# Kernel optimization log

Measured on AMD Instinct MI355X. Metric: run time of the kernel, lower is better.

Reference implementation:

```python
import jax, jax.numpy as jnp
import numpy as np

B, S, D, H = 8, 512, 1024, 16
DH = D // H
GAMMA = 0.1      # kl_gamma
KL_EPS = 1e-10
LN_EPS = 1e-5
SCALE = 1.0 / np.sqrt(DH).astype(np.float32)


def setup_inputs() -> dict:
    key = jax.random.key(0)
    ks = iter(jax.random.split(key, 32))
    rnd = lambda shape, s: jax.random.normal(next(ks), shape, jnp.float32) * s
    inp = {
        'title_features': rnd((B, S, D), 1.0),
        'content_features': rnd((B, S, D), 1.0),
    }
    for pre in ('t2c', 'c2t'):
        # small Q/K weights + bias 1.0 keep row-means of scores positive (log is defined)
        inp[pre + '_wq'] = rnd((D, D), 0.02); inp[pre + '_bq'] = jnp.ones((D,), jnp.float32)
        inp[pre + '_wk'] = rnd((D, D), 0.02); inp[pre + '_bk'] = jnp.ones((D,), jnp.float32)
        inp[pre + '_wv'] = rnd((D, D), 0.02); inp[pre + '_bv'] = jnp.zeros((D,), jnp.float32)
        inp[pre + '_wo'] = rnd((D, D), 0.02); inp[pre + '_bo'] = jnp.zeros((D,), jnp.float32)
    inp['gate_w'] = rnd((2 * D, D), 0.02)
    inp['gate_b'] = jnp.zeros((D,), jnp.float32)
    inp['ln_g'] = jnp.ones((D,), jnp.float32)
    inp['ln_b'] = jnpps = jnp.zeros((D,), jnp.float32)
    inp['ln_b'] = jnp.zeros((D,), jnp.float32)
    return inp


def _daa(q_in, k_in, v_in, wq, bq, wk, bk, wv, bv, wo, bo):
    """DivergenceAlignedAttention forward (eval mode, use_uniform_target=False)."""
    Bq, Sq, _ = q_in.shape
    Sk = k_in.shape[1]
    Q = (q_in @ wq + bq).reshape(Bq, Sq, H, DH)
    K = (k_in @ wk + bk).reshape(Bq, Sk, H, DH)
    V = (v_in @ wv + bv).reshape(Bq, Sk, H, DH)
    scores = jnp.einsum('bqhd,bkhd->bhqk', Q, K) * SCALE           # [B,H,Sq,Sk]
    tgt = jnp.mean(scores, axis=-1, keepdims=True)                 # row mean
    scores = scores + GAMMA * jnp.log(tgt + KL_EPS)                # fused KL term
    attn = jax.nn.softmax(scores, axis=-1)
    ctx = jnp.einsum('bhqk,bkhd->bqhd', attn, V).reshape(Bq, Sq, D)
    return ctx @ wo + bo


def _layer_norm(x, g, b):
    mu = jnp.mean(x, axis=-1, keepdims=True)
    var = jnp.mean(jnp.square(x - mu), axis=-1, keepdims=True)
    return g * (x - mu) / jnp.sqrt(var + LN_EPS) + b


def reference(title_features, content_features,
              t2c_wq, t2c_bq, t2c_wk, t2c_bk, t2c_wv, t2c_bv, t2c_wo, t2c_bo,
              c2t_wq, c2t_bq, c2t_wk, c2t_bk, c2t_wv, c2t_bv, c2t_wo, c2t_bo,
              gate_w, gate_b, ln_g, ln_b):
    t2c = _daa(content_features, title_features, title_features,
               t2c_wq, t2c_bq, t2c_wk, t2c_bk, t2c_wv, t2c_bv, t2c_wo, t2c_bo)
    c2t = _daa(title_features, content_features, content_features,
               c2t_wq, c2t_bq, c2t_wk, c2t_bk, c2t_wv, c2t_bv, c2t_wo, c2t_bo)
    gate_t = jax.nn.sigmoid(jnp.concatenate([title_features, t2c], axis=-1) @ gate_w + gate_b)
    gate_c = jax.nn.sigmoid(jnp.concatenate([content_features, c2t], axis=-1) @ gate_w + gate_b)
    fused_title = _layer_norm(gate_t * title_features + (1.0 - gate_t) * t2c, ln_g, ln_b)
    fused_content = _layer_norm(gate_c * content_features + (1.0 - gate_c) * c2t, ln_g, ln_b)
    return (fused_title, fused_content)
```

## Files before the change

kernel.cpp:

```cpp
#include <hip/hip_runtime.h>
#include <cstdint>
#include <cstddef>

typedef unsigned short ushort_t;
typedef unsigned int u32;
typedef __attribute__((ext_vector_type(8))) short bf16x8;
typedef __attribute__((ext_vector_type(4))) float f32x4;
typedef __attribute__((ext_vector_type(4))) unsigned short u16x4;

#define DEV static __device__ __forceinline__

DEV ushort_t f2bf(float f) {
  u32 x = __float_as_uint(f);
  x += 0x7fff + ((x >> 16) & 1);
  return (ushort_t)(x >> 16);
}
DEV float bf2f(ushort_t u) { return __uint_as_float(((u32)u) << 16); }

DEV void gload16(const ushort_t* g, ushort_t* l) {
  __builtin_amdgcn_global_load_lds(
      (const __attribute__((address_space(1))) void*)g,
      (__attribute__((address_space(3))) void*)l, 16, 0, 0);
}


__global__ __launch_bounds__(256) void cvt_inputs(
    const float* __restrict__ xa, const float* __restrict__ xb,
    ushort_t* __restrict__ oa, ushort_t* __restrict__ ob) {
  int i = blockIdx.x * 256 + threadIdx.x;
  f32x4 va = ((const f32x4*)xa)[i];
  f32x4 vb = ((const f32x4*)xb)[i];
  u16x4 ua, ub;
#pragma unroll
  for (int j = 0; j < 4; ++j) { ua[j] = f2bf(va[j]); ub[j] = f2bf(vb[j]); }
  ((u16x4*)oa)[i] = ua;
  ((u16x4*)ob)[i] = ub;
}

struct Src11 { const float* p[11]; };

__global__ __launch_bounds__(256) void transpose_cvt(
    Src11 srcs, ushort_t* __restrict__ WTall, ushort_t* __restrict__ WgT,
    ushort_t* __restrict__ WoBF) {
  const int z = blockIdx.z;
  if (z != 8 && blockIdx.y >= 32) return;
  const float* src = srcs.p[z];
  int tx = threadIdx.x & 31, ty = threadIdx.x >> 5;
  int n0 = blockIdx.x << 5, k0 = blockIdx.y << 5;
  if (z >= 9) {
    ushort_t* dst = WoBF + ((size_t)(z - 9) << 20);
#pragma unroll
    for (int i = 0; i < 4; ++i) {
      size_t off = (size_t)(k0 + ty + i * 8) * 1024 + n0 + tx;
      dst[off] = f2bf(src[off]);
    }
    return;
  }
  const int K = (z == 8) ? 2048 : 1024;
  ushort_t* dst = (z == 8) ? WgT : WTall + ((size_t)z << 20);
  __shared__ float t[32][33];
#pragma unroll
  for (int i = 0; i < 4; ++i)
    t[ty + i * 8][tx] = src[(size_t)(k0 + ty + i * 8) * 1024 + n0 + tx];
  __syncthreads();
#pragma unroll
  for (int i = 0; i < 4; ++i)
    dst[(size_t)(n0 + ty + i * 8) * K + k0 + tx] = f2bf(t[tx][ty + i * 8]);
}

__global__ __launch_bounds__(256) void gb2_kernel(
    const float* __restrict__ bo0, const float* __restrict__ bo1,
    const ushort_t* __restrict__ WgT, float* __restrict__ gb2) {
  const int wgl = blockIdx.x * 4 + (threadIdx.x >> 6);
  const int lane = threadIdx.x & 63;
  const int dir = wgl >> 10, n = wgl & 1023;
  const float* bo = dir ? bo1 : bo0;
  const ushort_t* wrow = WgT + ((size_t)n << 11) + 1024 + (lane << 4);
  float s = 0.f;
#pragma unroll
  for (int j = 0; j < 16; ++j) s += bo[(lane << 4) + j] * bf2f(wrow[j]);
#pragma unroll
  for (int d = 1; d < 64; d <<= 1) s += __shfl_xor(s, d, 64);
  if (lane == 0) gb2[wgl] = s;
}

__global__ __launch_bounds__(256, 3) void gemm_wp(
    const ushort_t* __restrict__ WgT, const ushort_t* __restrict__ WoBF,
    ushort_t* __restrict__ WpT) {
  __shared__ ushort_t As[128 * 64];
  __shared__ ushort_t Bs[128 * 64];
  const int tid = threadIdx.x;
  const int w = tid >> 6, lane = tid & 63;
  const int g = lane >> 4, c = lane & 15;
  const int wm = (w >> 1) << 6, wn = (w & 1) << 6;
  const int m0 = blockIdx.x << 7, n0 = blockIdx.y << 7;
  const int group = m0 >> 10;
  const int csw = (lane & 7) ^ (lane >> 3);

  f32x4 acc[4][4];
#pragma unroll
  for (int i = 0; i < 4; ++i)
#pragma unroll
    for (int j = 0; j < 4; ++j) acc[i][j] = f32x4{0.f, 0.f, 0.f, 0.f};

  for (int k0 = 0; k0 < 1024; k0 += 64) {
#pragma unroll
    for (int i = 0; i < 4; ++i) {
      const int chunk = (w << 2) + i;
      const int row = (chunk << 3) + (lane >> 3);
      gload16(WgT + ((size_t)((m0 + row) & 1023) << 11) + 1024 + k0 + (csw << 3),
              &As[(size_t)chunk << 9]);
      gload16(WoBF + ((size_t)group << 20) + ((size_t)(n0 + row) << 10) + k0 + (csw << 3),
              &Bs[(size_t)chunk << 9]);
    }
    __syncthreads();
    const int cg = c & 7;
#pragma unroll
    for (int ks = 0; ks < 2; ++ks) {
      bf16x8 af[4], bfr[4];
#pragma unroll
      for (int mi = 0; mi < 4; ++mi)
        af[mi] = *(const bf16x8*)&As[((wm + mi * 16 + c) << 6) +
                                     ((((ks << 2) | g) ^ cg) << 3)];
#pragma unroll
      for (int ni = 0; ni < 4; ++ni)
        bfr[ni] = *(const bf16x8*)&Bs[((wn + ni * 16 + c) << 6) +
                                      ((((ks << 2) | g) ^ cg) << 3)];
#pragma unroll
      for (int mi = 0; mi < 4; ++mi)
#pragma unroll
        for (int ni = 0; ni < 4; ++ni)
          acc[mi][ni] = __builtin_amdgcn_mfma_f32_16x16x32_bf16(
              af[mi], bfr[ni], acc[mi][ni], 0, 0, 0);
    }
    __syncthreads();
  }
#pragma unroll
  for (int ni = 0; ni < 4; ++ni) {
    const int n = n0 + wn + ni * 16 + c;
#pragma unroll
    for (int mi = 0; mi < 4; ++mi) {
      const int mb = m0 + wm + mi * 16 + (g << 2);
      f32x4 a = acc[mi][ni];
#pragma unroll
      for (int r = 0; r < 4; ++r)
        WpT[((size_t)group << 20) + ((size_t)((mb + r) & 1023) << 10) + n] = f2bf(a[r]);
    }
  }
}

enum { M_QKVG = 0, M_OG = 1 };
struct Bias8 { const float* p[8]; };

template <int MODE>
__global__ __launch_bounds__(256, 3) void gemm_kernel(
    const ushort_t* __restrict__ Aa, const ushort_t* __restrict__ Ab,
    const ushort_t* __restrict__ WTall, const ushort_t* __restrict__ WgT,
    const ushort_t* __restrict__ WpT, Bias8 bt, const float* __restrict__ gb2,
    ushort_t* __restrict__ outQ, ushort_t* __restrict__ gt) {
  __shared__ ushort_t As[128 * 64];
  __shared__ ushort_t Bs[128 * 64];
  const int tid = threadIdx.x;
  const int w = tid >> 6, lane = tid & 63;
  const int g = lane >> 4, c = lane & 15;
  const int wm = (w >> 1) << 6, wn = (w & 1) << 6;
  const int bid = (int)blockIdx.x;
  const int xcd = bid & 7, idx = bid >> 3;
  const int mt = (xcd << 3) + (idx & 7), nt = idx >> 3;
  const int m0 = mt << 7, n0 = nt << 7;
  const int group = m0 >> 12;
  const int nch = n0 >> 10;
  const int csw = (lane & 7) ^ (lane >> 3);

  const ushort_t* Asrc = (MODE == M_QKVG)
      ? ((group ? Ab : Aa) + ((size_t)(m0 & 4095) << 10))
      : (Aa + ((size_t)m0 << 10));

  const ushort_t* Bb;
  int bstr, bidx = -1;
  if (MODE == M_QKVG) {
    if (nch < 3) {
      bidx = group * 3 + nch;
      Bb = WTall + ((size_t)bidx << 20) + ((size_t)(n0 & 1023) << 10);
      bstr = 1024;
    } else {
      Bb = WgT + ((size_t)(n0 & 1023) << 11);
      bstr = 2048;
    }
  } else {
    if (nch == 0) {
      Bb = WTall + ((size_t)(6 + group) << 20) + ((size_t)n0 << 10);
      bstr = 1024;
    } else {
      Bb = WpT + ((size_t)group << 20) + ((size_t)(n0 & 1023) << 10);
      bstr = 1024;
    }
  }

  f32x4 acc[4][4];
#pragma unroll
  for (int i = 0; i < 4; ++i)
#pragma unroll
    for (int j = 0; j < 4; ++j) acc[i][j] = f32x4{0.f, 0.f, 0.f, 0.f};

  for (int k0 = 0; k0 < 1024; k0 += 64) {
#pragma unroll
    for (int i = 0; i < 4; ++i) {
      const int chunk = (w << 2) + i;
      const int row = (chunk << 3) + (lane >> 3);
      gload16(Asrc + ((size_t)row << 10) + k0 + (csw << 3), &As[(size_t)chunk << 9]);
      gload16(Bb + (size_t)row * bstr + k0 + (csw << 3), &Bs[(size_t)chunk << 9]);
    }
    __syncthreads();
    const int cg = c & 7;
#pragma unroll
    for (int ks = 0; ks < 2; ++ks) {
      bf16x8 af[4], bfr[4];
#pragma unroll
      for (int mi = 0; mi < 4; ++mi)
        af[mi] = *(const bf16x8*)&As[((wm + mi * 16 + c) << 6) +
                                     ((((ks << 2) | g) ^ cg) << 3)];
#pragma unroll
      for (int ni = 0; ni < 4; ++ni)
        bfr[ni] = *(const bf16x8*)&Bs[((wn + ni * 16 + c) << 6) +
                                      ((((ks << 2) | g) ^ cg) << 3)];
#pragma unroll
      for (int mi = 0; mi < 4; ++mi)
#pragma unroll
        for (int ni = 0; ni < 4; ++ni)
          acc[mi][ni] = __builtin_amdgcn_mfma_f32_16x16x32_bf16(
              af[mi], bfr[ni], acc[mi][ni], 0, 0, 0);
    }
    __syncthreads();
  }

#pragma unroll
  for (int ni = 0; ni < 4; ++ni) {
    const int n = n0 + wn + ni * 16 + c;
    const int nloc = n & 1023;
    float bv;
    if (MODE == M_QKVG)
      bv = (nch < 3) ? bt.p[bidx][nloc]
                     : bt.p[6][nloc] + gb2[(group << 10) + nloc];
    else
      bv = (nch == 0) ? bt.p[group][nloc] : 0.f;
#pragma unroll
    for (int mi = 0; mi < 4; ++mi) {
      const int mb = m0 + wm + mi * 16 + (g << 2);
      f32x4 a = acc[mi][ni];
      if (MODE == M_QKVG) {
        if (nch < 3) {
          const int mrow = mb & 4095, b = mrow >> 9, s = mrow & 511;
          const int h = nloc >> 6, d = nloc & 63;
          ushort_t* base = outQ + ((size_t)bidx << 22);
          if (bidx == 1 || bidx == 5) {
            u16x4 o;
#pragma unroll
            for (int r = 0; r < 4; ++r) o[r] = f2bf(a[r] + bv);
            *(u16x4*)&base[(((size_t)((b * 16 + h) * 64 + d)) << 9) + s] = o;
          } else {
#pragma unroll
            for (int r = 0; r < 4; ++r)
              base[(((size_t)((b * 16 + h) * 512 + s + r)) << 6) + d] = f2bf(a[r] + bv);
          }
        } else {
#pragma unroll
          for (int r = 0; r < 4; ++r)
            gt[((size_t)(mb + r) << 10) + nloc] = f2bf(a[r] + bv);
        }
      } else {
        if (nch == 0) {
#pragma unroll
          for (int r = 0; r < 4; ++r)
            outQ[((size_t)(mb + r) << 10) + nloc] = f2bf(a[r] + bv);
        } else {
#pragma unroll
          for (int r = 0; r < 4; ++r)
            gt[((size_t)(mb + r) << 10) + nloc] = f2bf(a[r]);
        }
      }
    }
  }
}

__global__ __launch_bounds__(256, 2) void attn_kernel(
    const ushort_t* __restrict__ QKV, ushort_t* __restrict__ ctx) {
  __shared__ ushort_t kv[2][8192];
  const int tid = threadIdx.x, w = tid >> 6, lane = tid & 63;
  const int g = lane >> 4, c = lane & 15, c7 = c & 7;
  const int bid = (int)blockIdx.x;
  const int wid = (bid & 7) * 256 + (bid >> 3);
  const int dir = wid >> 10;
  const int bh = (wid >> 3) & 127, qt = wid & 7;
  const int q0 = (qt << 6) + (w << 4);
  const int qs = dir ? 2 : 3, ks = dir ? 4 : 0, vs = dir ? 5 : 1;
  const ushort_t* Qb = QKV + ((size_t)qs << 22) + ((size_t)bh << 15);
  const ushort_t* Kb = QKV + ((size_t)ks << 22) + ((size_t)bh << 15);
  const ushort_t* Vb = QKV + ((size_t)vs << 22) + ((size_t)bh << 15);

  auto stageK = [&](int b, int kc) {
#pragma unroll
    for (int i = 0; i < 4; ++i) {
      int idx = tid + (i << 8);
      int r = idx >> 3, sl = idx & 7;
      int cs = sl ^ (r & 7);
      gload16(Kb + (((size_t)((kc << 7) + r)) << 6) + (cs << 3), &kv[b][idx << 3]);
    }
  };
  auto stageV = [&](int b, int vc) {
#pragma unroll
    for (int i = 0; i < 4; ++i) {
      int idx = tid + (i << 8);
      int r = idx >> 4, sl = idx & 15;
      int cs = sl ^ (r & 15);
      gload16(Vb + ((size_t)r << 9) + (vc << 7) + (cs << 3), &kv[b][idx << 3]);
    }
  };

  bf16x8 qf0 = *(const bf16x8*)&Qb[((q0 + c) << 6) + (g << 3)];
  bf16x8 qf1 = *(const bf16x8*)&Qb[((q0 + c) << 6) + 32 + (g << 3)];

  f32x4 s[32];
  float mx = -1e30f;
  int buf = 0;
  stageK(0, 0);
  __syncthreads();
#pragma unroll
  for (int kc = 0; kc < 4; ++kc) {
    if (kc < 3) stageK(buf ^ 1, kc + 1);
    __builtin_amdgcn_s_setprio(1);
#pragma unroll
    for (int t = 0; t < 8; ++t) {
      const ushort_t* base = &kv[buf][((t << 4) + c) << 6];
      bf16x8 a0 = *(const bf16x8*)&base[(g ^ c7) << 3];
      bf16x8 a1 = *(const bf16x8*)&base[((4 | g) ^ c7) << 3];
      f32x4 z = {0.f, 0.f, 0.f, 0.f};
      z = __builtin_amdgcn_mfma_f32_16x16x32_bf16(a0, qf0, z, 0, 0, 0);
      z = __builtin_amdgcn_mfma_f32_16x16x32_bf16(a1, qf1, z, 0, 0, 0);
      s[kc * 8 + t] = z;
      mx = fmaxf(mx, fmaxf(fmaxf(z[0], z[1]), fmaxf(z[2], z[3])));
    }
    __builtin_amdgcn_s_setprio(0);
    __syncthreads();
    buf ^= 1;
  }
  stageV(0, 0);
  buf = 0;

  mx = fmaxf(mx, __shfl_xor(mx, 16, 64));
  mx = fmaxf(mx, __shfl_xor(mx, 32, 64));
  const float SC = 0.125f;
  float sum = 0.f;
#pragma unroll
  for (int t = 0; t < 32; ++t) {
#pragma unroll
    for (int r = 0; r < 4; ++r) {
      float p = __expf((s[t][r] - mx) * SC);
      s[t][r] = p;
      sum += p;
    }
  }
  sum += __shfl_xor(sum, 16, 64);
  sum += __shfl_xor(sum, 32, 64);
  const float inv = 1.0f / sum;

  f32x4 pacc[4];
#pragma unroll
  for (int dt = 0; dt < 4; ++dt) pacc[dt] = f32x4{0.f, 0.f, 0.f, 0.f};
  const int s1 = ((g & 1) << 5) + c;
  const int s2 = s1 + 16;
  const bool hi = (g >> 1) != 0;
  __syncthreads();
#pragma unroll
  for (int vc = 0; vc < 4; ++vc) {
    if (vc < 3) stageV(buf ^ 1, vc + 1);
#pragma unroll
    for (int t2l = 0; t2l < 4; ++t2l) {
      const int t2 = (vc << 2) + t2l;
      u32 A0 = ((u32)f2bf(s[2 * t2][1]) << 16) | f2bf(s[2 * t2][0]);
      u32 A1p = ((u32)f2bf(s[2 * t2][3]) << 16) | f2bf(s[2 * t2][2]);
      u32 B0 = ((u32)f2bf(s[2 * t2 + 1][1]) << 16) | f2bf(s[2 * t2 + 1][0]);
      u32 B1 = ((u32)f2bf(s[2 * t2 + 1][3]) << 16) | f2bf(s[2 * t2 + 1][2]);
      u32 xA0 = (u32)__shfl((int)A0, s1, 64), xA1 = (u32)__shfl((int)A1p, s1, 64);
      u32 xB0 = (u32)__shfl((int)B0, s1, 64), xB1 = (u32)__shfl((int)B1, s1, 64);
      u32 yA0 = (u32)__shfl((int)A0, s2, 64), yA1 = (u32)__shfl((int)A1p, s2, 64);
      u32 yB0 = (u32)__shfl((int)B0, s2, 64), yB1 = (u32)__shfl((int)B1, s2, 64);
      union { bf16x8 v; u32 wd[4]; } pb;
      pb.wd[0] = hi ? xB0 : xA0;
      pb.wd[1] = hi ? xB1 : xA1;
      pb.wd[2] = hi ? yB0 : yA0;
      pb.wd[3] = hi ? yB1 : yA1;
      __builtin_amdgcn_s_setprio(1);
#pragma unroll
      for (int dt = 0; dt < 4; ++dt) {
        bf16x8 av = *(const bf16x8*)
            &kv[buf][(((dt << 4) + c) << 7) + ((((t2l << 2) | g) ^ c) << 3)];
        pacc[dt] = __builtin_amdgcn_mfma_f32_16x16x32_bf16(av, pb.v, pacc[dt], 0, 0, 0);
      }
      __builtin_amdgcn_s_setprio(0);
    }
    __syncthreads();
    buf ^= 1;
  }

  const int b = bh >> 4, h = bh & 15;
  size_t obase = ((size_t)dir << 22) + ((size_t)(b * 512 + q0 + c) << 10) + (h << 6);
#pragma unroll
  for (int dt = 0; dt < 4; ++dt) {
    u16x4 o;
#pragma unroll
    for (int r = 0; r < 4; ++r) o[r] = f2bf(pacc[dt][r] * inv);
    *(u16x4*)&ctx[obase + (dt << 4) + (g << 2)] = o;
  }
}

__global__ __launch_bounds__(256) void fuse_ln(
    const float* __restrict__ xt, const float* __restrict__ xc,
    const ushort_t* __restrict__ ao, const ushort_t* __restrict__ gt,
    const ushort_t* __restrict__ gp,
    const float* __restrict__ lng, const float* __restrict__ lnb,
    float* __restrict__ out) {
  const int row = blockIdx.x, dir = row >> 12, r = row & 4095;
  const float* x = (dir ? xc : xt) + ((size_t)r << 10);
  const ushort_t* a = ao + ((size_t)row << 10);
  const ushort_t* g1 = gt + ((size_t)row << 10);
  const ushort_t* g2 = gp + ((size_t)row << 10);
  float* o = out + ((size_t)row << 10);
  const int t = threadIdx.x, w = t >> 6, lane = t & 63;
  f32x4 xv = ((const f32x4*)x)[t];
  u16x4 av = ((const u16x4*)a)[t];
  u16x4 gv = ((const u16x4*)g1)[t];
  u16x4 pv = ((const u16x4*)g2)[t];
  f32x4 f;
  float sm = 0.f, sq = 0.f;
#pragma unroll
  for (int j = 0; j < 4; ++j) {
    float gate = 1.f / (1.f + __expf(-(bf2f(gv[j]) + bf2f(pv[j]))));
    float fv = gate * xv[j] + (1.f - gate) * bf2f(av[j]);
    f[j] = fv; sm += fv; sq += fv * fv;
  }
#pragma unroll
  for (int d = 1; d < 64; d <<= 1) {
    sm += __shfl_xor(sm, d, 64);
    sq += __shfl_xor(sq, d, 64);
  }
  __shared__ float ps[8];
  if (lane == 0) { ps[w] = sm; ps[4 + w] = sq; }
  __syncthreads();
  sm = ps[0] + ps[1] + ps[2] + ps[3];
  sq = ps[4] + ps[5] + ps[6] + ps[7];
  const float mu = sm * (1.f / 1024.f);
  const float var = sq * (1.f / 1024.f) - mu * mu;
  const float rstd = rsqrtf(var + 1e-5f);
  f32x4 lg = ((const f32x4*)lng)[t], lb = ((const f32x4*)lnb)[t];
  f32x4 ov;
#pragma unroll
  for (int j = 0; j < 4; ++j) ov[j] = lg[j] * (f[j] - mu) * rstd + lb[j];
  ((f32x4*)o)[t] = ov;
}

extern "C" void kernel_launch(void* const* d_in, const int* in_sizes, int n_in,
                              void* d_out, int out_size, void* d_ws, size_t ws_size,
                              hipStream_t stream) {
  (void)in_sizes; (void)n_in; (void)out_size; (void)ws_size;
  const float* title = (const float*)d_in[0];
  const float* content = (const float*)d_in[1];

  char* ws = (char*)d_ws;
  const size_t MB = 1u << 20;
  ushort_t* Xt    = (ushort_t*)(ws + 0 * MB);
  ushort_t* Xc    = (ushort_t*)(ws + 8 * MB);
  ushort_t* ctx   = (ushort_t*)(ws + 0 * MB);
  ushort_t* WTall = (ushort_t*)(ws + 16 * MB);
  ushort_t* WgT   = (ushort_t*)(ws + 32 * MB);
  ushort_t* QKV   = (ushort_t*)(ws + 36 * MB);
  ushort_t* ao    = (ushort_t*)(ws + 36 * MB);
  ushort_t* gpart = (ushort_t*)(ws + 52 * MB);
  ushort_t* gt    = (ushort_t*)(ws + 84 * MB);
  ushort_t* WoBF  = (ushort_t*)(ws + 100 * MB);
  ushort_t* WpT   = (ushort_t*)(ws + 104 * MB);
  float*    gb2   = (float*)   (ws + 108 * MB);

  cvt_inputs<<<4096, 256, 0, stream>>>(title, content, Xt, Xc);

  Src11 srcs;
  srcs.p[0] = (const float*)d_in[4];  srcs.p[1] = (const float*)d_in[6];
  srcs.p[2] = (const float*)d_in[10]; srcs.p[3] = (const float*)d_in[2];
  srcs.p[4] = (const float*)d_in[12]; srcs.p[5] = (const float*)d_in[14];
  srcs.p[6] = (const float*)d_in[8];  srcs.p[7] = (const float*)d_in[16];
  srcs.p[8] = (const float*)d_in[18];
  srcs.p[9] = (const float*)d_in[8];  srcs.p[10] = (const float*)d_in[16];
  transpose_cvt<<<dim3(32, 64, 11), 256, 0, stream>>>(srcs, WTall, WgT, WoBF);

  gb2_kernel<<<512, 256, 0, stream>>>((const float*)d_in[9], (const float*)d_in[17],
                                      WgT, gb2);
  gemm_wp<<<dim3(16, 8), 256, 0, stream>>>(WgT, WoBF, WpT);

  Bias8 bq;
  bq.p[0] = (const float*)d_in[5];  bq.p[1] = (const float*)d_in[7];
  bq.p[2] = (const float*)d_in[11]; bq.p[3] = (const float*)d_in[3];
  bq.p[4] = (const float*)d_in[13]; bq.p[5] = (const float*)d_in[15];
  bq.p[6] = (const float*)d_in[19]; bq.p[7] = nullptr;
  gemm_kernel<M_QKVG><<<2048, 256, 0, stream>>>(Xt, Xc, WTall, WgT, WpT, bq, gb2,
                                                QKV, gt);

  attn_kernel<<<2048, 256, 0, stream>>>(QKV, ctx);

  Bias8 bo;
  bo.p[0] = (const float*)d_in[9]; bo.p[1] = (const float*)d_in[17];
  for (int i = 2; i < 8; ++i) bo.p[i] = nullptr;
  gemm_kernel<M_OG><<<1024, 256, 0, stream>>>(ctx, nullptr, WTall, WgT, WpT, bo, gb2,
                                              ao, gpart);

  fuse_ln<<<8192, 256, 0, stream>>>(title, content, ao, gt, gpart,
                                    (const float*)d_in[20], (const float*)d_in[21],
                                    (float*)d_out);
}
```

Baseline: 226.4 us.

## Convert attention to online softmax over 64-key chunks with fused K/V staging

The attention kernel is restructured from a two-pass scheme, which held all 512 scores per lane in registers before running P·V, into a flash-style online softmax. Each 64-key chunk now computes its scores, rescales the running max, sum and accumulator, and feeds P·V immediately. K and V chunks are staged together into separate double-buffered LDS arrays. The goal is to cut register pressure so launch bounds can rise to 4 blocks per CU and K and V loads can overlap. In exchange it adds per-chunk rescaling work, cross-lane reductions, and twice as many barriers.

```diff
diff --git a/kernel.cpp b/kernel.cpp
--- a/kernel.cpp
+++ b/kernel.cpp
@@ -283,9 +283,10 @@
   }
 }
 
-__global__ __launch_bounds__(256, 2) void attn_kernel(
+__global__ __launch_bounds__(256, 4) void attn_kernel(
     const ushort_t* __restrict__ QKV, ushort_t* __restrict__ ctx) {
-  __shared__ ushort_t kv[2][8192];
+  __shared__ ushort_t Ks[2][4096];
+  __shared__ ushort_t Vs[2][4096];
   const int tid = threadIdx.x, w = tid >> 6, lane = tid & 63;
   const int g = lane >> 4, c = lane & 15, c7 = c & 7;
   const int bid = (int)blockIdx.x;
@@ -300,87 +301,90 @@
 
   auto stageK = [&](int b, int kc) {
 #pragma unroll
-    for (int i = 0; i < 4; ++i) {
+    for (int i = 0; i < 2; ++i) {
       int idx = tid + (i << 8);
       int r = idx >> 3, sl = idx & 7;
       int cs = sl ^ (r & 7);
-      gload16(Kb + (((size_t)((kc << 7) + r)) << 6) + (cs << 3), &kv[b][idx << 3]);
+      gload16(Kb + (((size_t)((kc << 6) + r)) << 6) + (cs << 3), &Ks[b][idx << 3]);
     }
   };
   auto stageV = [&](int b, int vc) {
 #pragma unroll
-    for (int i = 0; i < 4; ++i) {
+    for (int i = 0; i < 2; ++i) {
       int idx = tid + (i << 8);
-      int r = idx >> 4, sl = idx & 15;
-      int cs = sl ^ (r & 15);
-      gload16(Vb + ((size_t)r << 9) + (vc << 7) + (cs << 3), &kv[b][idx << 3]);
+      int r = idx >> 3, sl = idx & 7;
+      int cs = sl ^ (r & 7);
+      gload16(Vb + ((size_t)r << 9) + (vc << 6) + (cs << 3), &Vs[b][idx << 3]);
     }
   };
 
   bf16x8 qf0 = *(const bf16x8*)&Qb[((q0 + c) << 6) + (g << 3)];
   bf16x8 qf1 = *(const bf16x8*)&Qb[((q0 + c) << 6) + 32 + (g << 3)];
 
-  f32x4 s[32];
-  float mx = -1e30f;
-  int buf = 0;
+  const float SC = 0.125f;
+  float m = -1e30f, sum = 0.f;
+  f32x4 pacc[4];
+#pragma unroll
+  for (int dt = 0; dt < 4; ++dt) pacc[dt] = f32x4{0.f, 0.f, 0.f, 0.f};
+  const int s1 = ((g & 1) << 5) + c;
+  const int s2 = s1 + 16;
+  const bool hi = (g >> 1) != 0;
+
   stageK(0, 0);
+  stageV(0, 0);
   __syncthreads();
-#pragma unroll
-  for (int kc = 0; kc < 4; ++kc) {
-    if (kc < 3) stageK(buf ^ 1, kc + 1);
+
+#pragma unroll
+  for (int cc = 0; cc < 8; ++cc) {
+    const int buf = cc & 1;
+    if (cc < 7) { stageK(buf ^ 1, cc + 1); stageV(buf ^ 1, cc + 1); }
+
+    f32x4 st[4];
     __builtin_amdgcn_s_setprio(1);
 #pragma unroll
-    for (int t = 0; t < 8; ++t) {
-      const ushort_t* base = &kv[buf][((t << 4) + c) << 6];
+    for (int t = 0; t < 4; ++t) {
+      const ushort_t* base = &Ks[buf][((t << 4) + c) << 6];
       bf16x8 a0 = *(const bf16x8*)&base[(g ^ c7) << 3];
       bf16x8 a1 = *(const bf16x8*)&base[((4 | g) ^ c7) << 3];
       f32x4 z = {0.f, 0.f, 0.f, 0.f};
       z = __builtin_amdgcn_mfma_f32_16x16x32_bf16(a0, qf0, z, 0, 0, 0);
       z = __builtin_amdgcn_mfma_f32_16x16x32_bf16(a1, qf1, z, 0, 0, 0);
-      s[kc * 8 + t] = z;
-      mx = fmaxf(mx, fmaxf(fmaxf(z[0], z[1]), fmaxf(z[2], z[3])));
+      st[t] = z;
     }
     __builtin_amdgcn_s_setprio(0);
-    __syncthreads();
-    buf ^= 1;
-  }
-  stageV(0, 0);
-  buf = 0;
-
-  mx = fmaxf(mx, __shfl_xor(mx, 16, 64));
-  mx = fmaxf(mx, __shfl_xor(mx, 32, 64));
-  const float SC = 0.125f;
-  float sum = 0.f;
-#pragma unroll
-  for (int t = 0; t < 32; ++t) {
-#pragma unroll
-    for (int r = 0; r < 4; ++r) {
-      float p = __expf((s[t][r] - mx) * SC);
-      s[t][r] = p;
-      sum += p;
-    }
-  }
-  sum += __shfl_xor(sum, 16, 64);
-  sum += __shfl_xor(sum, 32, 64);
-  const float inv = 1.0f / sum;
-
-  f32x4 pacc[4];
-#pragma unroll
-  for (int dt = 0; dt < 4; ++dt) pacc[dt] = f32x4{0.f, 0.f, 0.f, 0.f};
-  const int s1 = ((g & 1) << 5) + c;
-  const int s2 = s1 + 16;
-  const bool hi = (g >> 1) != 0;
-  __syncthreads();
-#pragma unroll
-  for (int vc = 0; vc < 4; ++vc) {
-    if (vc < 3) stageV(buf ^ 1, vc + 1);
-#pragma unroll
-    for (int t2l = 0; t2l < 4; ++t2l) {
-      const int t2 = (vc << 2) + t2l;
-      u32 A0 = ((u32)f2bf(s[2 * t2][1]) << 16) | f2bf(s[2 * t2][0]);
-      u32 A1p = ((u32)f2bf(s[2 * t2][3]) << 16) | f2bf(s[2 * t2][2]);
-      u32 B0 = ((u32)f2bf(s[2 * t2 + 1][1]) << 16) | f2bf(s[2 * t2 + 1][0]);
-      u32 B1 = ((u32)f2bf(s[2 * t2 + 1][3]) << 16) | f2bf(s[2 * t2 + 1][2]);
+
+    float mx = fmaxf(fmaxf(st[0][0], st[0][1]), fmaxf(st[0][2], st[0][3]));
+#pragma unroll
+    for (int t = 1; t < 4; ++t)
+      mx = fmaxf(mx, fmaxf(fmaxf(st[t][0], st[t][1]), fmaxf(st[t][2], st[t][3])));
+    mx = fmaxf(mx, __shfl_xor(mx, 16, 64));
+    mx = fmaxf(mx, __shfl_xor(mx, 32, 64));
+    const float mn = fmaxf(m, mx);
+    const float scale = __expf((m - mn) * SC);
+    m = mn;
+    float ls = 0.f;
+#pragma unroll
+    for (int t = 0; t < 4; ++t)
+#pragma unroll
+      for (int r = 0; r < 4; ++r) {
+        float p = __expf((st[t][r] - mn) * SC);
+        st[t][r] = p;
+        ls += p;
+      }
+    ls += __shfl_xor(ls, 16, 64);
+    ls += __shfl_xor(ls, 32, 64);
+    sum = sum * scale + ls;
+#pragma unroll
+    for (int dt = 0; dt < 4; ++dt)
+#pragma unroll
+      for (int r = 0; r < 4; ++r) pacc[dt][r] *= scale;
+
+#pragma unroll
+    for (int u = 0; u < 2; ++u) {
+      u32 A0 = ((u32)f2bf(st[2 * u][1]) << 16) | f2bf(st[2 * u][0]);
+      u32 A1p = ((u32)f2bf(st[2 * u][3]) << 16) | f2bf(st[2 * u][2]);
+      u32 B0 = ((u32)f2bf(st[2 * u + 1][1]) << 16) | f2bf(st[2 * u + 1][0]);
+      u32 B1 = ((u32)f2bf(st[2 * u + 1][3]) << 16) | f2bf(st[2 * u + 1][2]);
       u32 xA0 = (u32)__shfl((int)A0, s1, 64), xA1 = (u32)__shfl((int)A1p, s1, 64);
       u32 xB0 = (u32)__shfl((int)B0, s1, 64), xB1 = (u32)__shfl((int)B1, s1, 64);
       u32 yA0 = (u32)__shfl((int)A0, s2, 64), yA1 = (u32)__shfl((int)A1p, s2, 64);
@@ -394,15 +398,15 @@
 #pragma unroll
       for (int dt = 0; dt < 4; ++dt) {
         bf16x8 av = *(const bf16x8*)
-            &kv[buf][(((dt << 4) + c) << 7) + ((((t2l << 2) | g) ^ c) << 3)];
+            &Vs[buf][(((dt << 4) + c) << 6) + ((((u << 2) | g) ^ c7) << 3)];
         pacc[dt] = __builtin_amdgcn_mfma_f32_16x16x32_bf16(av, pb.v, pacc[dt], 0, 0, 0);
       }
       __builtin_amdgcn_s_setprio(0);
     }
     __syncthreads();
-    buf ^= 1;
-  }
-
+  }
+
+  const float inv = 1.0f / sum;
   const int b = bh >> 4, h = bh & 15;
   size_t obase = ((size_t)dir << 22) + ((size_t)(b * 512 + q0 + c) << 10) + (h << 6);
 #pragma unroll
```

Result: no change. 224.3 us (-0.9%).
